# Performance work log

Measured on AMD Instinct MI355X. Metric: run time of the kernel, lower is better.

The kernel has to match this reference:

```python
import jax, jax.numpy as jnp
import numpy as np

B, N, E, D, H = 128, 256, 1024, 128, 8
DK = D // H
NEG = -9e15

def _xavier(key, shape):
    lim = np.sqrt(6.0 / (shape[0] + shape[1]))
    return jax.random.uniform(key, shape, jnp.float32, -lim, lim)

def setup_inputs() -> dict:
    key = jax.random.key(0)
    ks = jax.random.split(key, 10)
    x = jax.random.normal(ks[0], (B, N, D), jnp.float32)
    mask = jax.random.randint(ks[1], (B, N), 0, 2) > 0
    mask = mask.at[:, 0].set(True)  # ensure no fully-masked molecule
    # unique (row, col) edges per molecule -> scatter .set matches torch index_put
    perm = jax.vmap(lambda k: jax.random.permutation(k, N * N)[:E])(jax.random.split(ks[2], B))
    edge_index = jnp.stack([perm // N, perm % N], axis=1).astype(jnp.int32)  # [B, 2, E]
    edge_attr = jax.random.normal(ks[3], (B, E, D), jnp.float32)
    return {
        "x": x, "mask": mask, "edge_index": edge_index, "edge_attr": edge_attr,
        "Wq": _xavier(ks[4], (D + 2, D)),
        "Wk": _xavier(ks[5], (D + 2, D)),
        "Wv": _xavier(ks[6], (D + 2, D)),
        "We_w": _xavier(ks[7], (D, D)),
        "We_b": jax.random.normal(ks[8], (D,), jnp.float32) * 0.02,
        "ln_g": jnp.ones((D,), jnp.float32),
        "ln_b": jnp.zeros((D,), jnp.float32),
    }

def reference(x, mask, edge_index, edge_attr, Wq, Wk, Wv, We_w, We_b, ln_g, ln_b):
    rows, cols = edge_index[:, 0, :], edge_index[:, 1, :]  # [B, E]
    # per-molecule degree features (torch_geometric.degree per row/col)
    deg = lambda idx: jax.vmap(lambda r: jnp.zeros((N,), x.dtype).at[r].add(1.0))(idx)
    deg_r, deg_c = deg(rows), deg(cols)
    x_new = jnp.concatenate([x, deg_r[..., None], deg_c[..., None]], axis=-1)  # [B,N,D+2]
    # edge bias: linear -> mean over features -> scatter into [B,N,N]
    edge_feats = (edge_attr @ We_w + We_b).mean(axis=-1)  # [B, E]
    edge_bias = jax.vmap(lambda r, c, f: jnp.zeros((N, N), x.dtype).at[r, c].set(f))(rows, cols, edge_feats)
    q = (x_new @ Wq).reshape(B, N, H, DK).transpose(0, 2, 1, 3)
    k = (x_new @ Wk).reshape(B, N, H, DK).transpose(0, 2, 1, 3)
    v = (x_new @ Wv).reshape(B, N, H, DK).transpose(0, 2, 1, 3)
    scores = jnp.einsum('bhqd,bhkd->bhqk', q, k) / np.sqrt(DK).astype(x.dtype)
    # mask keys first, then add edge bias (matches torch op order)
    scores = jnp.where(mask[:, None, None, :], scores, NEG) + edge_bias[:, None, :, :]
    attn = jax.nn.softmax(scores, axis=-1)  # dropout is identity in eval
    out = jnp.einsum('bhqk,bhkd->bhqd', attn, v).transpose(0, 2, 1, 3).reshape(B, N, D)
    out = out + x
    mu = out.mean(axis=-1, keepdims=True)
    var = out.var(axis=-1, keepdims=True)
    return (out - mu) / jnp.sqrt(var + 1e-6) * ln_g + ln_b
```

## Files before the change

### kernel.cpp

```cpp
#include <hip/hip_runtime.h>
#include <stdint.h>

#define NB 128
#define NN 256
#define NE 1024
#define ND 128
#define NH 8
#define NDK 16
#define NEGV -9.0e15f

typedef unsigned short u16;
typedef unsigned int u32;
typedef unsigned char u8;
typedef __attribute__((ext_vector_type(8))) short short8;
typedef __attribute__((ext_vector_type(4))) float float4v;
typedef __attribute__((ext_vector_type(2))) float f32x2;

__device__ __forceinline__ float bf2f(u16 u) { return __uint_as_float(((u32)u) << 16); }
__device__ __forceinline__ u16 f2bf(float f) {
    u32 u = __float_as_uint(f);
    u += 0x7fffu + ((u >> 16) & 1u);
    return (u16)(u >> 16);
}
__device__ __forceinline__ float ldf(const void* p, size_t i, int f32) {
    return f32 ? ((const float*)p)[i] : bf2f(((const u16*)p)[i]);
}
__device__ __forceinline__ void stf(void* p, size_t i, int f32, float v) {
    if (f32) ((float*)p)[i] = v;
    else ((u16*)p)[i] = f2bf(v);
}
__device__ __forceinline__ void unpack8(uint4 a, float* o) {
    o[0] = bf2f(a.x & 0xffff); o[1] = bf2f(a.x >> 16);
    o[2] = bf2f(a.y & 0xffff); o[3] = bf2f(a.y >> 16);
    o[4] = bf2f(a.z & 0xffff); o[5] = bf2f(a.z >> 16);
    o[6] = bf2f(a.w & 0xffff); o[7] = bf2f(a.w >> 16);
}
__device__ __forceinline__ f32x2 bfpair(u32 w) {
    return (f32x2){__uint_as_float(w << 16), __uint_as_float(w & 0xffff0000u)};
}
__device__ __forceinline__ u32 pk_bf(float a, float b) {
    return ((__float_as_uint(a) + 0x8000u) >> 16) |
           ((__float_as_uint(b) + 0x8000u) & 0xffff0000u);
}
union Pack8 { u16 u[8]; u32 w[4]; short8 v; };

__global__ __launch_bounds__(256) void k_detect(const u16* x16, const u8* m8, int* flags) {
    __shared__ u32 sev[256], sg1[256], smx[256];
    int tid = threadIdx.x;
    u32 ev = 0;
    for (int i = tid * 128; i < tid * 128 + 128; ++i) {
        u32 e = (x16[i] >> 7) & 0xffu;
        ev |= (e >= 0xC2u) ? 1u : 0u;
    }
    u32 g1 = 0, mx = 0;
    for (int i = 0; i < 16; ++i) {
        int idx = tid * 16 + i;
        u32 bv = m8[idx];
        if ((idx & 3) == 1) g1 |= bv;
        mx = mx > bv ? mx : bv;
    }
    sev[tid] = ev; sg1[tid] = g1; smx[tid] = mx;
    __syncthreads();
    for (int s = 128; s > 0; s >>= 1) {
        if (tid < s) {
            sev[tid] |= sev[tid + s];
            sg1[tid] |= sg1[tid + s];
            smx[tid] = smx[tid] > smx[tid + s] ? smx[tid] : smx[tid + s];
        }
        __syncthreads();
    }
    if (tid == 0) {
        flags[0] = sev[0] ? 1 : 0;
        flags[1] = (sg1[0] == 0) ? 4 : ((smx[0] <= 1u) ? 1 : 2);
    }
}

__global__ __launch_bounds__(64) void k_wmean(const void* Wew, const void* Web,
                                              const int* flags, float* wmean) {
    int k = blockIdx.x, lane = threadIdx.x;
    int f32 = flags[0];
    const void* src = (k < 128) ? Wew : Web;
    size_t base = (k < 128) ? (size_t)k * ND : 0;
    float s = ldf(src, base + lane, f32) + ldf(src, base + lane + 64, f32);
#pragma unroll
    for (int off = 32; off; off >>= 1) s += __shfl_xor(s, off, 64);
    if (lane == 0) wmean[k] = s * (1.0f / ND);
}

__global__ __launch_bounds__(256) void k_efeat(const void* ea, const float* wmean,
                                               const int* flags, float* featsE) {
    __shared__ __align__(16) float swm[132];
    int tid = threadIdx.x;
    int f32 = flags[0];
    if (tid <= ND) swm[tid] = wmean[tid];
    __syncthreads();
    int sub = tid & 15, grp = tid >> 4;
    size_t eidx = (size_t)blockIdx.x * 16 + grp;
    const float4* wv = (const float4*)&swm[sub * 8];
    float4 w0 = wv[0], w1 = wv[1];
    size_t base = eidx * ND + sub * 8;
    float part;
    if (f32) {
        const float4* p = (const float4*)((const float*)ea + base);
        float4 a0 = p[0], a1 = p[1];
        part = a0.x * w0.x + a0.y * w0.y + a0.z * w0.z + a0.w * w0.w +
               a1.x * w1.x + a1.y * w1.y + a1.z * w1.z + a1.w * w1.w;
    } else {
        uint4 a = *(const uint4*)((const u16*)ea + base);
        float xv[8];
        unpack8(a, xv);
        part = xv[0] * w0.x + xv[1] * w0.y + xv[2] * w0.z + xv[3] * w0.w +
               xv[4] * w1.x + xv[5] * w1.y + xv[6] * w1.z + xv[7] * w1.w;
    }
    part += __shfl_xor(part, 1);
    part += __shfl_xor(part, 2);
    part += __shfl_xor(part, 4);
    part += __shfl_xor(part, 8);
    if (sub == 0) featsE[eidx] = part + swm[ND];
}

__global__ __launch_bounds__(256) void k_csr(const int* ei, const float* featsE,
                                             float* degr, float* degc, int* rowstartG,
                                             u16* colsG, float* featsG) {
    __shared__ int cr[NN], cc[NN], offs[NN], rs[NN + 1];
    int b = blockIdx.x, tid = threadIdx.x;
    cr[tid] = 0; cc[tid] = 0;
    __syncthreads();
    const int* rows = ei + (size_t)b * 2 * NE;
    const int* cols = rows + NE;
    for (int e = tid; e < NE; e += 256) {
        atomicAdd(&cr[rows[e]], 1);
        atomicAdd(&cc[cols[e]], 1);
    }
    __syncthreads();
    degr[b * NN + tid] = (float)cr[tid];
    degc[b * NN + tid] = (float)cc[tid];
    if (tid == 0) {
        int a = 0;
        for (int n = 0; n < NN; ++n) { rs[n] = a; a += cr[n]; }
        rs[NN] = a;
    }
    __syncthreads();
    offs[tid] = rs[tid];
    rowstartG[b * (NN + 1) + tid] = rs[tid];
    if (tid == 0) rowstartG[b * (NN + 1) + NN] = rs[NN];
    __syncthreads();
    for (int e = tid; e < NE; e += 256) {
        int r = rows[e];
        int pos = atomicAdd(&offs[r], 1);
        colsG[(size_t)b * NE + pos] = (u16)cols[e];
        featsG[(size_t)b * NE + pos] = featsE[(size_t)b * NE + e];
    }
}

__global__ __launch_bounds__(64) void k_packB(const void* Wq, const void* Wk,
                                              const void* Wv, const int* flags, u16* WP) {
    int kT = blockIdx.x / 24, nT = blockIdx.x % 24;
    int lane = threadIdx.x;
    int col = lane & 15, quad = lane >> 4;
    int n = nT * 16 + col;
    int mat = n >> 7, nm = n & 127;
    const void* W = (mat == 0) ? Wq : (mat == 1) ? Wk : Wv;
    int f32 = flags[0];
    Pack8 c;
#pragma unroll
    for (int j = 0; j < 8; ++j) {
        int k = kT * 32 + quad * 8 + j;
        c.u[j] = (k < 130) ? f2bf(ldf(W, (size_t)k * ND + nm, f32)) : (u16)0;
    }
    *(short8*)(WP + ((size_t)(kT * 24 + nT) * 64 + lane) * 8) = c.v;
}

__global__ __launch_bounds__(256) void k_gemm(const void* x, const float* degr,
                                              const float* degc, const u16* WP,
                                              const int* flags, u16* qw, u16* kw,
                                              u16* vw, u16* vt) {
    int tid = threadIdx.x;
    int w = tid >> 6, lane = tid & 63;
    int quad = lane >> 4, col = lane & 15;
    int m0 = blockIdx.x * 64 + w * 16;
    int row = m0 + col;
    int f32 = flags[0];

    float4v acc[24];
#pragma unroll
    for (int t = 0; t < 24; ++t) acc[t] = (float4v){0.f, 0.f, 0.f, 0.f};

    const short8* wp = (const short8*)WP;
    for (int kT = 0; kT < 5; ++kT) {
        short8 a;
        if (kT < 4) {
            if (!f32) {
                a = *(const short8*)((const u16*)x + (size_t)row * ND + kT * 32 + quad * 8);
            } else {
                const float* xf = (const float*)x + (size_t)row * ND + kT * 32 + quad * 8;
                Pack8 c;
#pragma unroll
                for (int j = 0; j < 8; ++j) c.u[j] = f2bf(xf[j]);
                a = c.v;
            }
        } else {
            Pack8 c;
#pragma unroll
            for (int j = 0; j < 8; ++j) c.u[j] = 0;
            if (quad == 0) {
                c.u[0] = f2bf(degr[row]);
                c.u[1] = f2bf(degc[row]);
            }
            a = c.v;
        }
#pragma unroll
        for (int nT = 0; nT < 24; ++nT) {
            short8 bfr = wp[(size_t)(kT * 24 + nT) * 64 + lane];
            acc[nT] = __builtin_amdgcn_mfma_f32_16x16x32_bf16(a, bfr, acc[nT], 0, 0, 0);
        }
    }
    int bb = m0 >> 8;
    int nodebase = (m0 & 255) + quad * 4;
#pragma unroll
    for (int nT = 0; nT < 16; ++nT) {
        int h = nT & 7;
        u16* O = (nT < 8) ? qw : kw;
        float sc = (nT < 8) ? 0.25f : 1.0f;
        size_t base = ((size_t)bb * NH + h) * NN + nodebase;
#pragma unroll
        for (int reg = 0; reg < 4; ++reg)
            O[(base + reg) * NDK + col] = f2bf(acc[nT][reg] * sc);
    }
#pragma unroll
    for (int nT = 16; nT < 24; ++nT) {
        int h = nT - 16;
        size_t base = ((size_t)bb * NH + h) * NN + nodebase;
#pragma unroll
        for (int reg = 0; reg < 4; ++reg)
            vw[(base + reg) * NDK + col] = f2bf(acc[nT][reg]);
        u32 lo = (u32)f2bf(acc[nT][0]) | ((u32)f2bf(acc[nT][1]) << 16);
        u32 hi = (u32)f2bf(acc[nT][2]) | ((u32)f2bf(acc[nT][3]) << 16);
        *(uint2*)(vt + (((size_t)bb * NH + h) * NDK + col) * NN + nodebase) = make_uint2(lo, hi);
    }
}

__global__ __launch_bounds__(256, 4) void k_attn(const u16* qg, const u16* kg,
                                              const u16* vw, const u16* vt,
                                              const void* mask, const int* flags,
                                              const int* rowstartG, const u16* colsG,
                                              const float* featsG, void* out) {
    __shared__ __align__(16) u16 Ks[NN][24];
    __shared__ __align__(16) u16 Vs[NDK][264];
    __shared__ __align__(16) float mb[NN];
    __shared__ __align__(16) float Of[NN * 17];
    __shared__ float lbuf[NN];
    int h = blockIdx.x, b = blockIdx.y, tid = threadIdx.x;
    int wv = tid >> 6, lane = tid & 63;
    int col = lane & 15, g = lane >> 4;
    int f32 = flags[0], mw = flags[1];
    size_t hb = ((size_t)b * NH + h) * NN;
    int e0 = rowstartG[b * (NN + 1) + tid];
    int e1 = rowstartG[b * (NN + 1) + tid + 1];
    {
        const uint4* src = (const uint4*)(kg + (hb + tid) * NDK);
        uint4 a0 = src[0], a1 = src[1];
        uint4* dst = (uint4*)&Ks[tid][0];
        dst[0] = a0; dst[1] = a1;
    }
    {
        int dk = tid >> 4, chunk = tid & 15;
        const uint4* src = (const uint4*)(vt + ((size_t)(b * NH + h) * NDK + dk) * NN + chunk * 16);
        uint4 a0 = src[0], a1 = src[1];
        uint4* dst = (uint4*)&Vs[dk][chunk * 16];
        dst[0] = a0; dst[1] = a1;
    }
    {
        size_t mi = (size_t)b * NN + tid;
        bool mv;
        if (mw == 4)      mv = ((const u32*)mask)[mi] != 0;
        else if (mw == 2) mv = ((const u16*)mask)[mi] != 0;
        else              mv = ((const u8*)mask)[mi] != 0;
        mb[tid] = mv ? 0.0f : NEGV;
    }
    short8 qf[4];
#pragma unroll
    for (int qt = 0; qt < 4; ++qt) {
        int qtabs = wv * 4 + qt;
        short8 qv = {0, 0, 0, 0, 0, 0, 0, 0};
        if (g < 2)
            qv = *(const short8*)(qg + (hb + qtabs * 16 + col) * NDK + 8 * g);
        qf[qt] = qv;
    }
    __syncthreads();

    float4v outv[4];
    float lpart[4];
#pragma unroll
    for (int qt = 0; qt < 4; ++qt) {
        outv[qt] = (float4v){0.f, 0.f, 0.f, 0.f};
        lpart[qt] = 0.f;
    }

    for (int kt = 0; kt < 16; ++kt) {
        short8 kf = {0, 0, 0, 0, 0, 0, 0, 0};
        if (g < 2) kf = *(const short8*)&Ks[kt * 16 + col][8 * g];
        Pack8 vv;
        {
            uint2 t2 = *(const uint2*)&Vs[col][kt * 16 + 4 * g];
            vv.w[0] = t2.x; vv.w[1] = t2.y; vv.w[2] = 0; vv.w[3] = 0;
        }
        float4 mb4 = *(const float4*)&mb[kt * 16 + 4 * g];
        float4v cin = (float4v){mb4.x, mb4.y, mb4.z, mb4.w};
#pragma unroll
        for (int qt = 0; qt < 4; ++qt) {
            float4v s4 = __builtin_amdgcn_mfma_f32_16x16x32_bf16(kf, qf[qt], cin, 0, 0, 0);
            float p0 = __expf(fminf(s4[0], 60.f));
            float p1 = __expf(fminf(s4[1], 60.f));
            float p2 = __expf(fminf(s4[2], 60.f));
            float p3 = __expf(fminf(s4[3], 60.f));
            lpart[qt] += (p0 + p1) + (p2 + p3);
            Pack8 pp;
            pp.w[0] = pk_bf(p0, p1);
            pp.w[1] = pk_bf(p2, p3);
            pp.w[2] = 0; pp.w[3] = 0;
            outv[qt] = __builtin_amdgcn_mfma_f32_16x16x32_bf16(pp.v, vv.v, outv[qt], 0, 0, 0);
        }
    }
#pragma unroll
    for (int qt = 0; qt < 4; ++qt) {
        float l = lpart[qt];
        l += __shfl_xor(l, 16);
        l += __shfl_xor(l, 32);
        if (g == 0) lbuf[(wv * 4 + qt) * 16 + col] = l;
        int q0 = (wv * 4 + qt) * 16 + 4 * g;
#pragma unroll
        for (int reg = 0; reg < 4; ++reg)
            Of[(q0 + reg) * 17 + col] = outv[qt][reg];
    }
    __syncthreads();

    float lfin = lbuf[tid];
    f32x2 r[8];
#pragma unroll
    for (int j = 0; j < 8; ++j)
        r[j] = (f32x2){Of[tid * 17 + 2 * j], Of[tid * 17 + 2 * j + 1]};
    {
        const uint4* qp = (const uint4*)(qg + (hb + tid) * NDK);
        uint4 qa_ = qp[0], qb_ = qp[1];
        f32x2 qr[8];
        qr[0] = bfpair(qa_.x); qr[1] = bfpair(qa_.y);
        qr[2] = bfpair(qa_.z); qr[3] = bfpair(qa_.w);
        qr[4] = bfpair(qb_.x); qr[5] = bfpair(qb_.y);
        qr[6] = bfpair(qb_.z); qr[7] = bfpair(qb_.w);
        for (int e = e0; e < e1; ++e) {
            int c = colsG[(size_t)b * NE + e];
            float f = featsG[(size_t)b * NE + e];
            const u32* kcw = (const u32*)&Ks[c][0];
            f32x2 s2 = qr[0] * bfpair(kcw[0]);
            s2 += qr[1] * bfpair(kcw[1]); s2 += qr[2] * bfpair(kcw[2]);
            s2 += qr[3] * bfpair(kcw[3]); s2 += qr[4] * bfpair(kcw[4]);
            s2 += qr[5] * bfpair(kcw[5]); s2 += qr[6] * bfpair(kcw[6]);
            s2 += qr[7] * bfpair(kcw[7]);
            float s = s2.x + s2.y + mb[c];
            float dl = __expf(fminf(s + f, 60.f)) - __expf(fminf(s, 60.f));
            lfin += dl;
            const uint4* vp = (const uint4*)(vw + (hb + c) * NDK);
            uint4 v0 = vp[0], v1 = vp[1];
            f32x2 d2 = (f32x2){dl, dl};
            r[0] += d2 * bfpair(v0.x); r[1] += d2 * bfpair(v0.y);
            r[2] += d2 * bfpair(v0.z); r[3] += d2 * bfpair(v0.w);
            r[4] += d2 * bfpair(v1.x); r[5] += d2 * bfpair(v1.y);
            r[6] += d2 * bfpair(v1.z); r[7] += d2 * bfpair(v1.w);
        }
    }
    float inv = 1.0f / lfin;
    size_t obase = ((size_t)(b * NN + tid)) * ND + h * NDK;
    if (f32) {
        float4* op = (float4*)((float*)out + obase);
#pragma unroll
        for (int jj = 0; jj < 4; ++jj) {
            float4 w;
            w.x = r[2 * jj].x * inv;     w.y = r[2 * jj].y * inv;
            w.z = r[2 * jj + 1].x * inv; w.w = r[2 * jj + 1].y * inv;
            op[jj] = w;
        }
    } else {
        u16* op = (u16*)out + obase;
        Pack8 pa, pb;
#pragma unroll
        for (int jj = 0; jj < 4; ++jj) {
            pa.u[2 * jj]     = f2bf(r[jj].x * inv);
            pa.u[2 * jj + 1] = f2bf(r[jj].y * inv);
            pb.u[2 * jj]     = f2bf(r[jj + 4].x * inv);
            pb.u[2 * jj + 1] = f2bf(r[jj + 4].y * inv);
        }
        *(uint4*)op = *(uint4*)&pa.w[0];
        *(uint4*)(op + 8) = *(uint4*)&pb.w[0];
    }
}

__global__ __launch_bounds__(256) void k_ln(void* out, const void* x, const void* g,
                                            const void* be, const int* flags) {
    int f32 = flags[0];
    int tid = threadIdx.x, wv = tid >> 6, lane = tid & 63;
    int row = blockIdx.x * 4 + wv;
    size_t base = (size_t)row * ND;
    float v0 = ldf(out, base + lane, f32) + ldf(x, base + lane, f32);
    float v1 = ldf(out, base + lane + 64, f32) + ldf(x, base + lane + 64, f32);
    float s = v0 + v1, ss = v0 * v0 + v1 * v1;
#pragma unroll
    for (int off = 32; off; off >>= 1) {
        s += __shfl_xor(s, off, 64);
        ss += __shfl_xor(ss, off, 64);
    }
    float mu = s * (1.0f / ND);
    float var = ss * (1.0f / ND) - mu * mu;
    float rs = rsqrtf(var + 1e-6f);
    float o0 = (v0 - mu) * rs * ldf(g, lane, f32) + ldf(be, lane, f32);
    float o1 = (v1 - mu) * rs * ldf(g, lane + 64, f32) + ldf(be, lane + 64, f32);
    stf(out, base + lane, f32, o0);
    stf(out, base + lane + 64, f32, o1);
}

extern "C" void kernel_launch(void* const* d_in, const int* in_sizes, int n_in,
                              void* d_out, int out_size, void* d_ws, size_t ws_size,
                              hipStream_t stream) {
    const void* x = d_in[0];
    const void* mask = d_in[1];
    const int* ei = (const int*)d_in[2];
    const void* ea = d_in[3];
    const void* Wq = d_in[4];
    const void* Wk = d_in[5];
    const void* Wv = d_in[6];
    const void* Wew = d_in[7];
    const void* Web = d_in[8];
    const void* lng = d_in[9];
    const void* lnb = d_in[10];

    char* ws = (char*)d_ws;
    size_t off = 0;
    int* flags = (int*)(ws + off);       off += 256;
    float* wmean = (float*)(ws + off);   off += 1024;
    float* degr = (float*)(ws + off);    off += (size_t)NB * NN * 4;
    float* degc = (float*)(ws + off);    off += (size_t)NB * NN * 4;
    int* rowstart = (int*)(ws + off);    off += (size_t)NB * (NN + 1) * 4 + 512;
    u16* colsG = (u16*)(ws + off);       off += (size_t)NB * NE * 2;
    float* featsG = (float*)(ws + off);  off += (size_t)NB * NE * 4;
    float* featsE = (float*)(ws + off);  off += (size_t)NB * NE * 4;
    u16* WP = (u16*)(ws + off);          off += (size_t)5 * 24 * 64 * 8 * 2;
    const size_t qkv_elems = (size_t)NB * NH * NN * NDK;
    u16* qw = (u16*)(ws + off);          off += qkv_elems * 2;
    u16* kw = (u16*)(ws + off);          off += qkv_elems * 2;
    u16* vw = (u16*)(ws + off);          off += qkv_elems * 2;
    u16* vt = (u16*)(ws + off);          off += qkv_elems * 2;

    k_detect<<<1, 256, 0, stream>>>((const u16*)x, (const u8*)mask, flags);
    k_wmean<<<129, 64, 0, stream>>>(Wew, Web, flags, wmean);
    k_efeat<<<(NB * NE) / 16, 256, 0, stream>>>(ea, wmean, flags, featsE);
    k_csr<<<NB, 256, 0, stream>>>(ei, featsE, degr, degc, rowstart, colsG, featsG);
    k_packB<<<120, 64, 0, stream>>>(Wq, Wk, Wv, flags, WP);
    k_gemm<<<(NB * NN) / 64, 256, 0, stream>>>(x, degr, degc, WP, flags, qw, kw, vw, vt);
    k_attn<<<dim3(NH, NB), 256, 0, stream>>>(qw, kw, vw, vt, mask, flags, rowstart,
                                             colsG, featsG, d_out);
    k_ln<<<(NB * NN) / 4, 256, 0, stream>>>(d_out, x, lng, lnb, flags);
}
```

Baseline: 208.8 us.

## Vectorize detect loads, batch attn prologue loads, prefetch next edge in sparse loop

The detect kernel now reads x and mask with 16-byte vector loads instead of scalar element loads. In the attention kernel, all global loads (K, V, mask, and the q row) are issued before any LDS stores, so their latencies overlap. The q-row load is moved from the edge-correction phase into the prologue. The per-row edge correction loop software-prefetches the next edge's column, feature and V row, hiding gather latency at the cost of extra live registers.

```diff
diff --git a/kernel.cpp b/kernel.cpp
--- a/kernel.cpp
+++ b/kernel.cpp
@@ -48,16 +48,30 @@
     __shared__ u32 sev[256], sg1[256], smx[256];
     int tid = threadIdx.x;
     u32 ev = 0;
-    for (int i = tid * 128; i < tid * 128 + 128; ++i) {
-        u32 e = (x16[i] >> 7) & 0xffu;
-        ev |= (e >= 0xC2u) ? 1u : 0u;
+    const uint4* xv = (const uint4*)(x16 + tid * 128);
+#pragma unroll
+    for (int i = 0; i < 16; ++i) {
+        uint4 a = xv[i];
+        u32 w[4] = {a.x, a.y, a.z, a.w};
+#pragma unroll
+        for (int j = 0; j < 4; ++j) {
+            ev |= ((((w[j] & 0xffffu) >> 7) & 0xffu) >= 0xC2u) ? 1u : 0u;
+            ev |= ((((w[j] >> 16) >> 7) & 0xffu) >= 0xC2u) ? 1u : 0u;
+        }
     }
     u32 g1 = 0, mx = 0;
-    for (int i = 0; i < 16; ++i) {
-        int idx = tid * 16 + i;
-        u32 bv = m8[idx];
-        if ((idx & 3) == 1) g1 |= bv;
-        mx = mx > bv ? mx : bv;
+    {
+        uint4 m = *(const uint4*)(m8 + tid * 16);
+        u32 w[4] = {m.x, m.y, m.z, m.w};
+#pragma unroll
+        for (int j = 0; j < 4; ++j) {
+            u32 b0 = w[j] & 0xffu, b1 = (w[j] >> 8) & 0xffu;
+            u32 b2 = (w[j] >> 16) & 0xffu, b3 = w[j] >> 24;
+            g1 |= b1;
+            u32 ma = b0 > b1 ? b0 : b1, mbv = b2 > b3 ? b2 : b3;
+            u32 mc = ma > mbv ? ma : mbv;
+            mx = mx > mc ? mx : mc;
+        }
     }
     sev[tid] = ev; sg1[tid] = g1; smx[tid] = mx;
     __syncthreads();
@@ -257,26 +271,26 @@
     size_t hb = ((size_t)b * NH + h) * NN;
     int e0 = rowstartG[b * (NN + 1) + tid];
     int e1 = rowstartG[b * (NN + 1) + tid + 1];
-    {
-        const uint4* src = (const uint4*)(kg + (hb + tid) * NDK);
-        uint4 a0 = src[0], a1 = src[1];
-        uint4* dst = (uint4*)&Ks[tid][0];
-        dst[0] = a0; dst[1] = a1;
-    }
-    {
-        int dk = tid >> 4, chunk = tid & 15;
-        const uint4* src = (const uint4*)(vt + ((size_t)(b * NH + h) * NDK + dk) * NN + chunk * 16);
-        uint4 a0 = src[0], a1 = src[1];
-        uint4* dst = (uint4*)&Vs[dk][chunk * 16];
-        dst[0] = a0; dst[1] = a1;
-    }
+    const uint4* ksrc = (const uint4*)(kg + (hb + tid) * NDK);
+    uint4 ka0 = ksrc[0], ka1 = ksrc[1];
+    int dk = tid >> 4, chunk = tid & 15;
+    const uint4* vsrc = (const uint4*)(vt + ((size_t)(b * NH + h) * NDK + dk) * NN + chunk * 16);
+    uint4 va0 = vsrc[0], va1 = vsrc[1];
+    bool mv;
     {
         size_t mi = (size_t)b * NN + tid;
-        bool mv;
         if (mw == 4)      mv = ((const u32*)mask)[mi] != 0;
         else if (mw == 2) mv = ((const u16*)mask)[mi] != 0;
         else              mv = ((const u8*)mask)[mi] != 0;
-        mb[tid] = mv ? 0.0f : NEGV;
+    }
+    f32x2 qr[8];
+    {
+        const uint4* qp = (const uint4*)(qg + (hb + tid) * NDK);
+        uint4 qa_ = qp[0], qb_ = qp[1];
+        qr[0] = bfpair(qa_.x); qr[1] = bfpair(qa_.y);
+        qr[2] = bfpair(qa_.z); qr[3] = bfpair(qa_.w);
+        qr[4] = bfpair(qb_.x); qr[5] = bfpair(qb_.y);
+        qr[6] = bfpair(qb_.z); qr[7] = bfpair(qb_.w);
     }
     short8 qf[4];
 #pragma unroll
@@ -286,6 +300,13 @@
         if (g < 2)
             qv = *(const short8*)(qg + (hb + qtabs * 16 + col) * NDK + 8 * g);
         qf[qt] = qv;
+    }
+    {
+        uint4* kdst = (uint4*)&Ks[tid][0];
+        kdst[0] = ka0; kdst[1] = ka1;
+        uint4* vdst = (uint4*)&Vs[dk][chunk * 16];
+        vdst[0] = va0; vdst[1] = va1;
+        mb[tid] = mv ? 0.0f : NEGV;
     }
     __syncthreads();
 
@@ -340,33 +361,36 @@
 #pragma unroll
     for (int j = 0; j < 8; ++j)
         r[j] = (f32x2){Of[tid * 17 + 2 * j], Of[tid * 17 + 2 * j + 1]};
-    {
-        const uint4* qp = (const uint4*)(qg + (hb + tid) * NDK);
-        uint4 qa_ = qp[0], qb_ = qp[1];
-        f32x2 qr[8];
-        qr[0] = bfpair(qa_.x); qr[1] = bfpair(qa_.y);
-        qr[2] = bfpair(qa_.z); qr[3] = bfpair(qa_.w);
-        qr[4] = bfpair(qb_.x); qr[5] = bfpair(qb_.y);
-        qr[6] = bfpair(qb_.z); qr[7] = bfpair(qb_.w);
+    if (e0 < e1) {
+        const u16* colsB = colsG + (size_t)b * NE;
+        const float* featsB = featsG + (size_t)b * NE;
+        int c = colsB[e0];
+        float f = featsB[e0];
+        const uint4* vp0 = (const uint4*)(vw + (hb + c) * NDK);
+        uint4 v0 = vp0[0], v1 = vp0[1];
         for (int e = e0; e < e1; ++e) {
-            int c = colsG[(size_t)b * NE + e];
-            float f = featsG[(size_t)b * NE + e];
-            const u32* kcw = (const u32*)&Ks[c][0];
+            int cc_ = c; float ff_ = f;
+            uint4 w0 = v0, w1 = v1;
+            if (e + 1 < e1) {
+                c = colsB[e + 1];
+                f = featsB[e + 1];
+                const uint4* vp = (const uint4*)(vw + (hb + c) * NDK);
+                v0 = vp[0]; v1 = vp[1];
+            }
+            const u32* kcw = (const u32*)&Ks[cc_][0];
             f32x2 s2 = qr[0] * bfpair(kcw[0]);
             s2 += qr[1] * bfpair(kcw[1]); s2 += qr[2] * bfpair(kcw[2]);
             s2 += qr[3] * bfpair(kcw[3]); s2 += qr[4] * bfpair(kcw[4]);
             s2 += qr[5] * bfpair(kcw[5]); s2 += qr[6] * bfpair(kcw[6]);
             s2 += qr[7] * bfpair(kcw[7]);
-            float s = s2.x + s2.y + mb[c];
-            float dl = __expf(fminf(s + f, 60.f)) - __expf(fminf(s, 60.f));
+            float s = s2.x + s2.y + mb[cc_];
+            float dl = __expf(fminf(s + ff_, 60.f)) - __expf(fminf(s, 60.f));
             lfin += dl;
-            const uint4* vp = (const uint4*)(vw + (hb + c) * NDK);
-            uint4 v0 = vp[0], v1 = vp[1];
             f32x2 d2 = (f32x2){dl, dl};
-            r[0] += d2 * bfpair(v0.x); r[1] += d2 * bfpair(v0.y);
-            r[2] += d2 * bfpair(v0.z); r[3] += d2 * bfpair(v0.w);
-            r[4] += d2 * bfpair(v1.x); r[5] += d2 * bfpair(v1.y);
-            r[6] += d2 * bfpair(v1.z); r[7] += d2 * bfpair(v1.w);
+            r[0] += d2 * bfpair(w0.x); r[1] += d2 * bfpair(w0.y);
+            r[2] += d2 * bfpair(w0.z); r[3] += d2 * bfpair(w0.w);
+            r[4] += d2 * bfpair(w1.x); r[5] += d2 * bfpair(w1.y);
+            r[6] += d2 * bfpair(w1.z); r[7] += d2 * bfpair(w1.w);
         }
     }
     float inv = 1.0f / lfin;
```

New measurement: 209.5 us. About the same (+0.4%).
